# Performance work log

Measured on AMD Instinct MI355X. Metric: run time of the kernel, lower is better.

The kernel has to match this reference:

```python
import jax, jax.numpy as jnp
import numpy as np

B, N, I, O, R = 8, 1024, 256, 256, 8


def setup_inputs() -> dict:
    key = jax.random.key(0)
    k1, k2, k3 = jax.random.split(key, 3)
    x = jax.random.normal(k1, (B, N, I), dtype=jnp.float32)
    adj = jax.random.uniform(k2, (B, N, N, R), dtype=jnp.float32)  # soft adjacency [b, src, dst, r]
    weight = jax.random.normal(k3, (R, I, O), dtype=jnp.float32)   # per-relation transform
    return {"x": x, "adj": adj, "weight": weight}


def reference(x, adj, weight):
    # per-relation transformed features: [b, src, r, o]
    f = jnp.einsum('bni,rio->bnro', x, weight)
    # contraction over source nodes and relations, weighted by soft adjacency:
    # out[b, dst, o] = sum_{src, r} adj[b, src, dst, r] * f[b, src, r, o]
    out = jnp.einsum('bnro,bnmr->bmo', f, adj)
    # normalization: total incoming soft-edge weight per destination node
    denom = jnp.clip(adj.sum(axis=(1, 3)), 1e-16, None)  # [b, dst]
    return out / denom[..., None]
```

## Files before the change

kernel.cpp:

```cpp
#include <hip/hip_runtime.h>
#include <stdint.h>


typedef float          floatx4  __attribute__((ext_vector_type(4)));
typedef short          shortx8  __attribute__((ext_vector_type(8)));
typedef unsigned short ushortx4 __attribute__((ext_vector_type(4)));
typedef unsigned short ushortx8 __attribute__((ext_vector_type(8)));

__device__ __forceinline__ unsigned short f2bf(float f) {
  union { float f; unsigned int u; } v; v.f = f;
  unsigned int u = v.u + 0x7FFFu + ((v.u >> 16) & 1u);
  return (unsigned short)(u >> 16);
}

__device__ __forceinline__ void gload16(const void* g, void* l) {
  __builtin_amdgcn_global_load_lds((__attribute__((address_space(1))) void*)g,
                                   (__attribute__((address_space(3))) void*)l,
                                   16, 0, 0);
}

__global__ __launch_bounds__(256) void prep_xw(const float* __restrict__ x,
                                               const float* __restrict__ w,
                                               unsigned short* __restrict__ xbf,
                                               unsigned short* __restrict__ wt) {
  int bid = blockIdx.x;
  if (bid < 1024) {
    int t = bid * 256 + threadIdx.x;
    const float4* p = (const float4*)x + (size_t)t * 2;
    float4 a = p[0], b4 = p[1];
    ushortx8 o;
    o[0] = f2bf(a.x);  o[1] = f2bf(a.y);  o[2] = f2bf(a.z);  o[3] = f2bf(a.w);
    o[4] = f2bf(b4.x); o[5] = f2bf(b4.y); o[6] = f2bf(b4.z); o[7] = f2bf(b4.w);
    *(ushortx8*)(xbf + (size_t)t * 8) = o;
  } else {
    int id = (bid - 1024) * 256 + threadIdx.x;
    int r = id >> 16, i = (id >> 8) & 255, o = id & 255;
    float v = w[((size_t)(r * 256 + i) << 8) + o];
    wt[((size_t)(o * 8 + r) << 8) + i] = f2bf(v);
  }
}

__global__ __launch_bounds__(256) void k1_gemm(const unsigned short* __restrict__ xbf,
                                               const unsigned short* __restrict__ wt,
                                               unsigned short* __restrict__ ft) {
  int bid = blockIdx.x;
  int p0 = (bid & 15) * 128, q0 = (bid >> 4) * 128;
  int l = threadIdx.x & 63, w = threadIdx.x >> 6;
  int lr = l & 15, lg = l >> 4;
  int pw = p0 + (w >> 1) * 64, qw = q0 + (w & 1) * 64;

  floatx4 acc[4][4] = {};
#pragma unroll
  for (int ks = 0; ks < 8; ++ks) {
    shortx8 a[4], b[4];
#pragma unroll
    for (int pi = 0; pi < 4; ++pi)
      a[pi] = *(const shortx8*)(wt + (size_t)(pw + pi * 16 + lr) * 256 + ks * 32 + lg * 8);
#pragma unroll
    for (int qi = 0; qi < 4; ++qi)
      b[qi] = *(const shortx8*)(xbf + (size_t)(qw + qi * 16 + lr) * 256 + ks * 32 + lg * 8);
#pragma unroll
    for (int pi = 0; pi < 4; ++pi)
#pragma unroll
      for (int qi = 0; qi < 4; ++qi)
        acc[pi][qi] = __builtin_amdgcn_mfma_f32_16x16x32_bf16(a[pi], b[qi], acc[pi][qi], 0, 0, 0);
  }
#pragma unroll
  for (int pi = 0; pi < 4; ++pi) {
    int nbase = pw + pi * 16 + lg * 4;
    int o = nbase >> 3, rb = nbase & 7;
#pragma unroll
    for (int qi = 0; qi < 4; ++qi) {
      int m = qw + qi * 16 + lr;
      int b8 = m >> 10, src = m & 1023;
      ushortx4 h;
      h[0] = f2bf(acc[pi][qi][0]); h[1] = f2bf(acc[pi][qi][1]);
      h[2] = f2bf(acc[pi][qi][2]); h[3] = f2bf(acc[pi][qi][3]);
      *(ushortx4*)(ft + ((size_t)(b8 * 256 + o) << 13) + src * 8 + rb) = h;
    }
  }
}

#define BSZ (256 * 64)
#define ASZ (32 * 64)
__global__ __launch_bounds__(256, 2) void k2_gemm(const float* __restrict__ adj,
                                                  const unsigned short* __restrict__ ft,
                                                  float* __restrict__ pout,
                                                  float* __restrict__ dpart) {
  __shared__ __align__(16) unsigned short Blds[2 * BSZ];
  __shared__ __align__(16) unsigned short Alds[2 * ASZ];

  int bid = blockIdx.x;
  int b = bid & 7;
  int kc = (bid >> 3) & 1;
  int dst0 = (bid >> 4) * 32;

  int t = threadIdx.x, l = t & 63, w = t >> 6;
  int lr = l & 15, lg = l >> 4;

  int dst_l = l >> 1;
  int rh = (l & 1) * 4;
  int csw = (l & 7) ^ (l >> 3);

  const size_t adj_b = (size_t)b << 23;
  const unsigned short* ftb = ft + ((size_t)b << 21);
  int src_base = kc * 512;
  const int KT = 64;

  float dsum = 0.f;
  floatx4 acc[2][4] = {};
  float4 av[2];

  auto A_load = [&](int kt, float4* v) {
#pragma unroll
    for (int j = 0; j < 2; ++j) {
      int src_l = w + j * 4;
      v[j] = *(const float4*)(adj + adj_b + ((size_t)(src_base + kt * 8 + src_l) << 13)
                              + ((size_t)(dst0 + dst_l) << 3) + rh);
    }
  };
  auto A_store = [&](int buf, const float4* v) {
#pragma unroll
    for (int j = 0; j < 2; ++j) {
      int src_l = w + j * 4;
      float4 q = v[j];
      dsum += q.x + q.y + q.z + q.w;
      ushortx4 h;
      h[0] = f2bf(q.x); h[1] = f2bf(q.y); h[2] = f2bf(q.z); h[3] = f2bf(q.w);
      int slot = src_l ^ (dst_l & 7);
      *(ushortx4*)&Alds[buf * ASZ + dst_l * 64 + slot * 8 + rh] = h;
    }
  };
  auto B_stage = [&](int kt, int buf) {
    int kbase = (src_base + kt * 8) * 8;
#pragma unroll
    for (int i = 0; i < 8; ++i) {
      int orow = i * 32 + w * 8 + (l >> 3);
      const unsigned short* g = ftb + ((size_t)orow << 13) + kbase + (csw << 3);
      gload16(g, &Blds[buf * BSZ + (i * 32 + w * 8) * 64]);
    }
  };
  auto compute = [&](int buf) {
#pragma unroll
    for (int s = 0; s < 2; ++s) {
      int slotbase = s * 4 + lg;
      shortx8 af[2], bfr[4];
#pragma unroll
      for (int mi = 0; mi < 2; ++mi) {
        int arow = mi * 16 + lr;
        af[mi] = *(const shortx8*)&Alds[buf * ASZ + arow * 64 + ((slotbase ^ (arow & 7)) << 3)];
      }
#pragma unroll
      for (int ni = 0; ni < 4; ++ni) {
        int oc = w * 64 + ni * 16 + lr;
        bfr[ni] = *(const shortx8*)&Blds[buf * BSZ + oc * 64 + ((slotbase ^ (oc & 7)) << 3)];
      }
#pragma unroll
      for (int mi = 0; mi < 2; ++mi)
#pragma unroll
        for (int ni = 0; ni < 4; ++ni)
          acc[mi][ni] = __builtin_amdgcn_mfma_f32_16x16x32_bf16(af[mi], bfr[ni], acc[mi][ni], 0, 0, 0);
    }
  };

  A_load(0, av);
  B_stage(0, 0);
  A_store(0, av);
  __syncthreads();

  for (int kt = 0; kt < KT; ++kt) {
    int cur = kt & 1, nxt = cur ^ 1;
    bool has = (kt + 1) < KT;
    if (has) { A_load(kt + 1, av); B_stage(kt + 1, nxt); }
    compute(cur);
    if (has) A_store(nxt, av);
    __syncthreads();
  }

  float* dsf = (float*)Alds;
  dsf[t] = dsum;
  __syncthreads();
  if (t < 32) {
    float s = 0.f;
#pragma unroll
    for (int sl = 0; sl < 4; ++sl) {
      s += dsf[sl * 64 + t * 2];
      s += dsf[sl * 64 + t * 2 + 1];
    }
    dsf[256 + t] = s;
    dpart[kc * 8192 + (b << 10) + dst0 + t] = s;
  }
  __syncthreads();

#pragma unroll
  for (int mi = 0; mi < 2; ++mi) {
#pragma unroll
    for (int reg = 0; reg < 4; ++reg) {
      int row = dst0 + mi * 16 + lg * 4 + reg;
#pragma unroll
      for (int ni = 0; ni < 4; ++ni) {
        int col = w * 64 + ni * 16 + lr;
        pout[(size_t)kc * 2097152 + (((size_t)b << 10) + row) * 256 + col] = acc[mi][ni][reg];
      }
    }
  }
}

__global__ __launch_bounds__(256) void k3_reduce(const float* __restrict__ pout,
                                                 const float* __restrict__ dpart,
                                                 float* __restrict__ outp) {
  int bid = blockIdx.x;
  size_t base = (size_t)bid * 256 + threadIdx.x;
  float v = pout[base] + pout[2097152 + base];
  float d = dpart[bid] + dpart[8192 + bid];
  outp[base] = v / fmaxf(d, 1e-16f);
}

extern "C" void kernel_launch(void* const* d_in, const int* in_sizes, int n_in,
                              void* d_out, int out_size, void* d_ws, size_t ws_size,
                              hipStream_t stream) {
  const float* x   = (const float*)d_in[0];
  const float* adj = (const float*)d_in[1];
  const float* w   = (const float*)d_in[2];
  float* out = (float*)d_out;

  char* ws = (char*)d_ws;
  unsigned short* ft  = (unsigned short*)(ws);
  unsigned short* xbf = (unsigned short*)(ws + 33554432);
  unsigned short* wt  = (unsigned short*)(ws + 37748736);
  float* pout  = (float*)(ws + 38797312);
  float* dpart = (float*)(ws + 55574528);

  prep_xw<<<3072, 256, 0, stream>>>(x, w, xbf, wt);
  k1_gemm<<<1024, 256, 0, stream>>>(xbf, wt, ft);
  k2_gemm<<<512, 256, 0, stream>>>(adj, ft, pout, dpart);
  k3_reduce<<<8192, 256, 0, stream>>>(pout, dpart, out);
}
```

Measured before the change: 161.7 us.

## Replace split-K with output-column tiling and fuse normalization into k2

The adjacency GEMM no longer splits the source dimension into two halves that need a separate reduction kernel. Each block now covers the full source range for a 32×64 output tile and divides by the per-row adjacency sum in its epilogue. This removes the partial-output buffer, its readback and the k3 launch. In exchange, each block now reads the full adjacency slice for its destination rows, so adjacency traffic from memory or cache grows up to fourfold, and per-block MFMA work per LDS tile shrinks.

Measured after the change: 166.9 us. +3.2%, slower.

```diff
diff --git a/kernel.cpp b/kernel.cpp
--- a/kernel.cpp
+++ b/kernel.cpp
@@ -81,19 +81,19 @@
   }
 }
 
-#define BSZ (256 * 64)
+#define BSZ (64 * 64)
 #define ASZ (32 * 64)
-__global__ __launch_bounds__(256, 2) void k2_gemm(const float* __restrict__ adj,
+#define NKT 128
+__global__ __launch_bounds__(256, 4) void k2_gemm(const float* __restrict__ adj,
                                                   const unsigned short* __restrict__ ft,
-                                                  float* __restrict__ pout,
-                                                  float* __restrict__ dpart) {
+                                                  float* __restrict__ outp) {
   __shared__ __align__(16) unsigned short Blds[2 * BSZ];
   __shared__ __align__(16) unsigned short Alds[2 * ASZ];
 
   int bid = blockIdx.x;
   int b = bid & 7;
-  int kc = (bid >> 3) & 1;
-  int dst0 = (bid >> 4) * 32;
+  int o0 = ((bid >> 3) & 3) * 64;
+  int dst0 = (bid >> 5) * 32;
 
   int t = threadIdx.x, l = t & 63, w = t >> 6;
   int lr = l & 15, lg = l >> 4;
@@ -104,18 +104,16 @@
 
   const size_t adj_b = (size_t)b << 23;
   const unsigned short* ftb = ft + ((size_t)b << 21);
-  int src_base = kc * 512;
-  const int KT = 64;
 
   float dsum = 0.f;
-  floatx4 acc[2][4] = {};
+  floatx4 acc[2] = {};
   float4 av[2];
 
   auto A_load = [&](int kt, float4* v) {
 #pragma unroll
     for (int j = 0; j < 2; ++j) {
-      int src_l = w + j * 4;
-      v[j] = *(const float4*)(adj + adj_b + ((size_t)(src_base + kt * 8 + src_l) << 13)
+      int src = kt * 8 + w + j * 4;
+      v[j] = *(const float4*)(adj + adj_b + ((size_t)src << 13)
                               + ((size_t)(dst0 + dst_l) << 3) + rh);
     }
   };
@@ -132,34 +130,29 @@
     }
   };
   auto B_stage = [&](int kt, int buf) {
-    int kbase = (src_base + kt * 8) * 8;
-#pragma unroll
-    for (int i = 0; i < 8; ++i) {
-      int orow = i * 32 + w * 8 + (l >> 3);
-      const unsigned short* g = ftb + ((size_t)orow << 13) + kbase + (csw << 3);
-      gload16(g, &Blds[buf * BSZ + (i * 32 + w * 8) * 64]);
+    int kbase = kt * 64;
+#pragma unroll
+    for (int i = 0; i < 2; ++i) {
+      int orow = w * 16 + i * 8 + (l >> 3);
+      const unsigned short* g = ftb + ((size_t)(o0 + orow) << 13) + kbase + (csw << 3);
+      gload16(g, &Blds[buf * BSZ + (w * 16 + i * 8) * 64]);
     }
   };
   auto compute = [&](int buf) {
 #pragma unroll
     for (int s = 0; s < 2; ++s) {
       int slotbase = s * 4 + lg;
-      shortx8 af[2], bfr[4];
+      shortx8 af[2];
 #pragma unroll
       for (int mi = 0; mi < 2; ++mi) {
         int arow = mi * 16 + lr;
         af[mi] = *(const shortx8*)&Alds[buf * ASZ + arow * 64 + ((slotbase ^ (arow & 7)) << 3)];
       }
-#pragma unroll
-      for (int ni = 0; ni < 4; ++ni) {
-        int oc = w * 64 + ni * 16 + lr;
-        bfr[ni] = *(const shortx8*)&Blds[buf * BSZ + oc * 64 + ((slotbase ^ (oc & 7)) << 3)];
-      }
+      int brow = w * 16 + lr;
+      shortx8 bfr = *(const shortx8*)&Blds[buf * BSZ + brow * 64 + ((slotbase ^ (lr & 7)) << 3)];
 #pragma unroll
       for (int mi = 0; mi < 2; ++mi)
-#pragma unroll
-        for (int ni = 0; ni < 4; ++ni)
-          acc[mi][ni] = __builtin_amdgcn_mfma_f32_16x16x32_bf16(af[mi], bfr[ni], acc[mi][ni], 0, 0, 0);
+        acc[mi] = __builtin_amdgcn_mfma_f32_16x16x32_bf16(af[mi], bfr, acc[mi], 0, 0, 0);
     }
   };
 
@@ -168,9 +161,9 @@
   A_store(0, av);
   __syncthreads();
 
-  for (int kt = 0; kt < KT; ++kt) {
+  for (int kt = 0; kt < NKT; ++kt) {
     int cur = kt & 1, nxt = cur ^ 1;
-    bool has = (kt + 1) < KT;
+    bool has = (kt + 1) < NKT;
     if (has) { A_load(kt + 1, av); B_stage(kt + 1, nxt); }
     compute(cur);
     if (has) A_store(nxt, av);
@@ -188,7 +181,6 @@
       s += dsf[sl * 64 + t * 2 + 1];
     }
     dsf[256 + t] = s;
-    dpart[kc * 8192 + (b << 10) + dst0 + t] = s;
   }
   __syncthreads();
 
@@ -196,24 +188,13 @@
   for (int mi = 0; mi < 2; ++mi) {
 #pragma unroll
     for (int reg = 0; reg < 4; ++reg) {
-      int row = dst0 + mi * 16 + lg * 4 + reg;
-#pragma unroll
-      for (int ni = 0; ni < 4; ++ni) {
-        int col = w * 64 + ni * 16 + lr;
-        pout[(size_t)kc * 2097152 + (((size_t)b << 10) + row) * 256 + col] = acc[mi][ni][reg];
-      }
-    }
-  }
-}
-
-__global__ __launch_bounds__(256) void k3_reduce(const float* __restrict__ pout,
-                                                 const float* __restrict__ dpart,
-                                                 float* __restrict__ outp) {
-  int bid = blockIdx.x;
-  size_t base = (size_t)bid * 256 + threadIdx.x;
-  float v = pout[base] + pout[2097152 + base];
-  float d = dpart[bid] + dpart[8192 + bid];
-  outp[base] = v / fmaxf(d, 1e-16f);
+      int rowl = mi * 16 + lg * 4 + reg;
+      float dinv = 1.f / fmaxf(dsf[256 + rowl], 1e-16f);
+      int row = dst0 + rowl;
+      int col = o0 + w * 16 + lr;
+      outp[(((size_t)b << 10) + row) * 256 + col] = acc[mi][reg] * dinv;
+    }
+  }
 }
 
 extern "C" void kernel_launch(void* const* d_in, const int* in_sizes, int n_in,
@@ -228,11 +209,8 @@
   unsigned short* ft  = (unsigned short*)(ws);
   unsigned short* xbf = (unsigned short*)(ws + 33554432);
   unsigned short* wt  = (unsigned short*)(ws + 37748736);
-  float* pout  = (float*)(ws + 38797312);
-  float* dpart = (float*)(ws + 55574528);
 
   prep_xw<<<3072, 256, 0, stream>>>(x, w, xbf, wt);
   k1_gemm<<<1024, 256, 0, stream>>>(xbf, wt, ft);
-  k2_gemm<<<512, 256, 0, stream>>>(adj, ft, pout, dpart);
-  k3_reduce<<<8192, 256, 0, stream>>>(pout, dpart, out);
-}
+  k2_gemm<<<1024, 256, 0, stream>>>(adj, ft, out);
+}
```

## Retile k2 GEMM to 64x128 tiles with triple-buffered LDS pipeline

Applied to the files above, without the earlier changes.

Restructures the adjacency contraction kernel to use 512-thread blocks that each compute a 64-destination by 128-output tile, splitting the output dimension across two blocks. The single-stage double buffer becomes a three-buffer pipeline that prefetches two steps ahead. Raw s_waitcnt/s_barrier fences replace __syncthreads so outstanding global loads can stay in flight across the barrier. Each block now loads twice as much adjacency per output and reads half as much of the transformed features. The hand-written waitcnt counts are fragile and must match the number of loads issued per step.

Result: faster. 137.0 us (-15.3%).

```diff
diff --git a/kernel.cpp b/kernel.cpp
--- a/kernel.cpp
+++ b/kernel.cpp
@@ -18,6 +18,10 @@
                                    (__attribute__((address_space(3))) void*)l,
                                    16, 0, 0);
 }
+
+#define FENCE_KEEP4 asm volatile("s_waitcnt vmcnt(4) lgkmcnt(0)" ::: "memory")
+#define FENCE_ALL   asm volatile("s_waitcnt vmcnt(0) lgkmcnt(0)" ::: "memory")
+#define MEMFENCE    asm volatile("" ::: "memory")
 
 __global__ __launch_bounds__(256) void prep_xw(const float* __restrict__ x,
                                                const float* __restrict__ w,
@@ -81,48 +85,50 @@
   }
 }
 
-#define BSZ (256 * 64)
-#define ASZ (32 * 64)
-__global__ __launch_bounds__(256, 2) void k2_gemm(const float* __restrict__ adj,
+#define ASZ (64 * 64)
+#define BSZ (128 * 64)
+__global__ __launch_bounds__(512, 4) void k2_gemm(const float* __restrict__ adj,
                                                   const unsigned short* __restrict__ ft,
                                                   float* __restrict__ pout,
                                                   float* __restrict__ dpart) {
-  __shared__ __align__(16) unsigned short Blds[2 * BSZ];
-  __shared__ __align__(16) unsigned short Alds[2 * ASZ];
+  __shared__ __align__(16) unsigned short Alds[3 * ASZ];
+  __shared__ __align__(16) unsigned short Blds[3 * BSZ];
 
   int bid = blockIdx.x;
   int b = bid & 7;
-  int kc = (bid >> 3) & 1;
-  int dst0 = (bid >> 4) * 32;
+  int o0 = ((bid >> 3) & 1) * 128;
+  int kc = (bid >> 4) & 1;
+  int dst0 = (bid >> 5) * 64;
 
   int t = threadIdx.x, l = t & 63, w = t >> 6;
   int lr = l & 15, lg = l >> 4;
-
-  int dst_l = l >> 1;
-  int rh = (l & 1) * 4;
+  int wm = w >> 2, wo = w & 3;
+
+  int dst_l = (t >> 1) & 63;
+  int rh = (t & 1) * 4;
+  int sA = t >> 7;
   int csw = (l & 7) ^ (l >> 3);
 
   const size_t adj_b = (size_t)b << 23;
   const unsigned short* ftb = ft + ((size_t)b << 21);
-  int src_base = kc * 512;
-  const int KT = 64;
+  const int src_base = kc * 512;
 
   float dsum = 0.f;
-  floatx4 acc[2][4] = {};
-  float4 av[2];
+  floatx4 acc[2][2] = {};
+  float4 av0[2], av1[2];
 
   auto A_load = [&](int kt, float4* v) {
 #pragma unroll
     for (int j = 0; j < 2; ++j) {
-      int src_l = w + j * 4;
-      v[j] = *(const float4*)(adj + adj_b + ((size_t)(src_base + kt * 8 + src_l) << 13)
+      int src = src_base + kt * 8 + sA + j * 4;
+      v[j] = *(const float4*)(adj + adj_b + ((size_t)src << 13)
                               + ((size_t)(dst0 + dst_l) << 3) + rh);
     }
   };
   auto A_store = [&](int buf, const float4* v) {
 #pragma unroll
     for (int j = 0; j < 2; ++j) {
-      int src_l = w + j * 4;
+      int src_l = sA + j * 4;
       float4 q = v[j];
       dsum += q.x + q.y + q.z + q.w;
       ushortx4 h;
@@ -134,72 +140,92 @@
   auto B_stage = [&](int kt, int buf) {
     int kbase = (src_base + kt * 8) * 8;
 #pragma unroll
-    for (int i = 0; i < 8; ++i) {
-      int orow = i * 32 + w * 8 + (l >> 3);
-      const unsigned short* g = ftb + ((size_t)orow << 13) + kbase + (csw << 3);
-      gload16(g, &Blds[buf * BSZ + (i * 32 + w * 8) * 64]);
+    for (int i = 0; i < 2; ++i) {
+      int orow = w * 16 + i * 8 + (l >> 3);
+      const unsigned short* g = ftb + ((size_t)(o0 + orow) << 13) + kbase + (csw << 3);
+      gload16(g, &Blds[buf * BSZ + (w * 16 + i * 8) * 64]);
     }
   };
   auto compute = [&](int buf) {
 #pragma unroll
     for (int s = 0; s < 2; ++s) {
       int slotbase = s * 4 + lg;
-      shortx8 af[2], bfr[4];
+      shortx8 af[2], bfr[2];
 #pragma unroll
       for (int mi = 0; mi < 2; ++mi) {
-        int arow = mi * 16 + lr;
+        int arow = wm * 32 + mi * 16 + lr;
         af[mi] = *(const shortx8*)&Alds[buf * ASZ + arow * 64 + ((slotbase ^ (arow & 7)) << 3)];
       }
 #pragma unroll
-      for (int ni = 0; ni < 4; ++ni) {
-        int oc = w * 64 + ni * 16 + lr;
-        bfr[ni] = *(const shortx8*)&Blds[buf * BSZ + oc * 64 + ((slotbase ^ (oc & 7)) << 3)];
+      for (int ni = 0; ni < 2; ++ni) {
+        int brow = wo * 32 + ni * 16 + lr;
+        bfr[ni] = *(const shortx8*)&Blds[buf * BSZ + brow * 64 + ((slotbase ^ (brow & 7)) << 3)];
       }
 #pragma unroll
       for (int mi = 0; mi < 2; ++mi)
 #pragma unroll
-        for (int ni = 0; ni < 4; ++ni)
+        for (int ni = 0; ni < 2; ++ni)
           acc[mi][ni] = __builtin_amdgcn_mfma_f32_16x16x32_bf16(af[mi], bfr[ni], acc[mi][ni], 0, 0, 0);
     }
   };
 
-  A_load(0, av);
+#define STEP(kt, C0, C1, C2, RIN, ROUT, ISS, ST)                       \
+  {                                                                    \
+    if (ISS) { A_load((kt) + 2, ROUT); B_stage((kt) + 2, C2); }        \
+    if (ST)  A_store(C1, RIN);                                         \
+    compute(C0);                                                       \
+    if (ST) {                                                          \
+      if (ISS) { FENCE_KEEP4; } else { FENCE_ALL; }                    \
+      __builtin_amdgcn_s_barrier();                                    \
+      MEMFENCE;                                                        \
+    }                                                                  \
+  }
+
   B_stage(0, 0);
-  A_store(0, av);
+  A_load(0, av0);
+  A_load(1, av1);
+  B_stage(1, 1);
+  A_store(0, av0);
+  FENCE_KEEP4;
+  __builtin_amdgcn_s_barrier();
+  MEMFENCE;
+
+  for (int kt0 = 0; kt0 < 60; kt0 += 6) {
+    STEP(kt0 + 0, 0, 1, 2, av1, av0, 1, 1);
+    STEP(kt0 + 1, 1, 2, 0, av0, av1, 1, 1);
+    STEP(kt0 + 2, 2, 0, 1, av1, av0, 1, 1);
+    STEP(kt0 + 3, 0, 1, 2, av0, av1, 1, 1);
+    STEP(kt0 + 4, 1, 2, 0, av1, av0, 1, 1);
+    STEP(kt0 + 5, 2, 0, 1, av0, av1, 1, 1);
+  }
+  STEP(60, 0, 1, 2, av1, av0, 1, 1);
+  STEP(61, 1, 2, 0, av0, av1, 1, 1);
+  STEP(62, 2, 0, 1, av1, av0, 0, 1);
+  STEP(63, 0, 1, 2, av0, av1, 0, 0);
+#undef STEP
   __syncthreads();
-
-  for (int kt = 0; kt < KT; ++kt) {
-    int cur = kt & 1, nxt = cur ^ 1;
-    bool has = (kt + 1) < KT;
-    if (has) { A_load(kt + 1, av); B_stage(kt + 1, nxt); }
-    compute(cur);
-    if (has) A_store(nxt, av);
-    __syncthreads();
-  }
 
   float* dsf = (float*)Alds;
   dsf[t] = dsum;
   __syncthreads();
-  if (t < 32) {
+  if (t < 64) {
     float s = 0.f;
 #pragma unroll
     for (int sl = 0; sl < 4; ++sl) {
-      s += dsf[sl * 64 + t * 2];
-      s += dsf[sl * 64 + t * 2 + 1];
-    }
-    dsf[256 + t] = s;
+      s += dsf[sl * 128 + t * 2];
+      s += dsf[sl * 128 + t * 2 + 1];
+    }
     dpart[kc * 8192 + (b << 10) + dst0 + t] = s;
   }
-  __syncthreads();
 
 #pragma unroll
   for (int mi = 0; mi < 2; ++mi) {
 #pragma unroll
     for (int reg = 0; reg < 4; ++reg) {
-      int row = dst0 + mi * 16 + lg * 4 + reg;
-#pragma unroll
-      for (int ni = 0; ni < 4; ++ni) {
-        int col = w * 64 + ni * 16 + lr;
+      int row = dst0 + wm * 32 + mi * 16 + lg * 4 + reg;
+#pragma unroll
+      for (int ni = 0; ni < 2; ++ni) {
+        int col = o0 + wo * 32 + ni * 16 + lr;
         pout[(size_t)kc * 2097152 + (((size_t)b << 10) + row) * 256 + col] = acc[mi][ni][reg];
       }
     }
@@ -233,6 +259,6 @@
 
   prep_xw<<<3072, 256, 0, stream>>>(x, w, xbf, wt);
   k1_gemm<<<1024, 256, 0, stream>>>(xbf, wt, ft);
-  k2_gemm<<<512, 256, 0, stream>>>(adj, ft, pout, dpart);
+  k2_gemm<<<512, 512, 0, stream>>>(adj, ft, pout, dpart);
   k3_reduce<<<8192, 256, 0, stream>>>(pout, dpart, out);
 }
```
